# Performance work log

Hardware: AMD Instinct MI355X
Metric: run time of the kernel (lower is better)

The kernel has to match this reference:

```python
import jax, jax.numpy as jnp
import numpy as np

NUM_CLUSTER = 64
NUM_HEAD = 8
EMBED = 512
B, L = 32, 256
H = EMBED // NUM_HEAD  # 64


def setup_inputs() -> dict:
    key = jax.random.key(0)
    ks = jax.random.split(key, 8)
    inputs = jax.random.normal(ks[0], (B, L, EMBED), dtype=jnp.float32)
    emissions = jax.random.normal(ks[1], (B, L, NUM_CLUSTER), dtype=jnp.float32)
    targets = jax.random.randint(ks[2], (B, L), 0, NUM_CLUSTER)
    masks = jnp.ones((B, L), dtype=bool)
    scale = 1.0 / np.sqrt(H)
    W1 = jax.random.normal(ks[3], (NUM_CLUSTER, H), dtype=jnp.float32) * scale
    b1 = jax.random.normal(ks[4], (NUM_CLUSTER,), dtype=jnp.float32) * 0.01
    W2 = jax.random.normal(ks[5], (NUM_CLUSTER, H), dtype=jnp.float32) * scale
    b2 = jax.random.normal(ks[6], (NUM_CLUSTER,), dtype=jnp.float32) * 0.01
    start_transitions = jax.random.uniform(ks[7], (NUM_CLUSTER,), minval=-0.1, maxval=0.1, dtype=jnp.float32)
    end_transitions = jax.random.uniform(jax.random.fold_in(key, 99), (NUM_CLUSTER,), minval=-0.1, maxval=0.1, dtype=jnp.float32)
    return {"inputs": inputs, "emissions": emissions, "targets": targets, "masks": masks,
            "W1": W1, "b1": b1, "W2": W2, "b2": b2,
            "start_transitions": start_transitions, "end_transitions": end_transitions}


def reference(inputs, emissions, targets, masks, W1, b1, W2, b2, start_transitions, end_transitions):
    # batch_first -> time-major (L, B, ...)
    x = jnp.transpose(inputs, (1, 0, 2))          # [L,B,D]
    em = jnp.transpose(emissions, (1, 0, 2))      # [L,B,K]
    tg = targets.T                                # [L,B]
    mk = masks.T                                  # [L,B] bool
    Ls, Bs, D = x.shape
    K = start_transitions.shape[0]

    # biaffine per-step transitions: [L,B,K,K]
    flat = x.reshape(Ls, Bs, NUM_HEAD, D // NUM_HEAD)        # [L,B,C,H]
    e1 = jnp.einsum('lbch,kh->lbck', flat, W1) + b1          # [L,B,C,K]
    e2 = jnp.einsum('lbch,kh->lbck', flat, W2) + b2
    T = jnp.einsum('lbck,lbcj->lbkj', e1, e2)                # sum over channels

    mf = mk.astype(em.dtype)
    barange = jnp.arange(Bs)

    # ---- numerator (gold path score) ----
    score = start_transitions[tg[0]] + em[0, barange, tg[0]]
    steps = jnp.arange(1, Ls)[:, None]                       # [L-1,1]
    trans_sel = T[steps, barange[None, :], tg[:-1], tg[1:]]  # [L-1,B]
    em_sel = em[steps, barange[None, :], tg[1:]]             # [L-1,B]
    score = score + jnp.sum((trans_sel + em_sel) * mf[1:], axis=0)
    seq_ends = mk.astype(jnp.int32).sum(axis=0) - 1
    last_tags = tg[seq_ends, barange]
    numerator = score + end_transitions[last_tags]

    # ---- denominator (log partition) via scan ----
    def step(s, inp):
        Ti, emi, mki = inp                                   # [B,K,K],[B,K],[B]
        nxt = jax.nn.logsumexp(s[:, :, None] + Ti + emi[:, None, :], axis=1)
        s = jnp.where(mki[:, None], nxt, s)
        return s, None

    s0 = start_transitions + em[0]                           # [B,K]
    sF, _ = jax.lax.scan(step, s0, (T[1:], em[1:], mk[1:]))
    denominator = jax.nn.logsumexp(sF + end_transitions, axis=1)

    return numerator - denominator
```

## Files before the change

kernel.cpp:

```cpp
#include <hip/hip_runtime.h>
#include <hip/hip_bf16.h>
#include <cstddef>
#include <cstdint>

constexpr int Bn = 32;
constexpr int Ln = 256;
constexpr int SCH = 16;
constexpr int NCH = 16;

using bf16 = __hip_bfloat16;
typedef __bf16 bfv8 __attribute__((ext_vector_type(8)));
typedef float f32x16 __attribute__((ext_vector_type(16)));

union FragU {
  bfv8 f;
  uint4 q;
  uint2 d[2];
  unsigned short u[8];
};

__device__ inline unsigned int packbf2(float a, float b) {
  unsigned short lo = __builtin_bit_cast(unsigned short, __float2bfloat16(a));
  unsigned short hi = __builtin_bit_cast(unsigned short, __float2bfloat16(b));
  return (unsigned int)lo | ((unsigned int)hi << 16);
}
__device__ inline float bfbits2f(unsigned short v) {
  return __builtin_bit_cast(float, ((unsigned int)v) << 16);
}

__global__ __launch_bounds__(256) void chunk_kernel(
    const float* __restrict__ x, const float* __restrict__ W1,
    const float* __restrict__ b1, const float* __restrict__ W2,
    const float* __restrict__ b2, const float* __restrict__ em,
    const int* __restrict__ tg, bf16* __restrict__ cM,
    float* __restrict__ cOff, float* __restrict__ pnum) {
  const int blk = blockIdx.x;
  const int b = blk & (Bn - 1);
  const int c = blk >> 5;
  const int tid = threadIdx.x;
  const int lane = tid & 63;
  const int wv = tid >> 6;
  const int ti = wv >> 1, tj = wv & 1;
  const int l31 = lane & 31, h5 = lane >> 5;

  __shared__ __align__(16) unsigned short e1s[SCH * 512];
  __shared__ __align__(16) unsigned short e2s[SCH * 512];
  __shared__ __align__(16) unsigned short Rt[2][64 * 68];
  __shared__ __align__(16) unsigned short Pt[2][64 * 68];
  __shared__ __align__(16) float ems[SCH * 64];
  __shared__ float wvred[4], wvred2[4];

  const int t0g = c * SCH;

  {
    const float4* src = (const float4*)(em + ((size_t)b * Ln + t0g) * 64);
    ((float4*)ems)[tid] = src[tid];
  }

  FragU fxa[4];
  {
    const float* xbase = x + ((size_t)(b * Ln + t0g)) * 512;
    const int m = wv * 32 + l31;
    const float* xrow = xbase + (size_t)(m >> 3) * 512 + (m & 7) * 64;
#pragma unroll
    for (int kb = 0; kb < 4; ++kb) {
      const float4 x0 = *(const float4*)(xrow + kb * 16 + h5 * 8);
      const float4 x1 = *(const float4*)(xrow + kb * 16 + h5 * 8 + 4);
      fxa[kb].d[0] = make_uint2(packbf2(x0.x, x0.y), packbf2(x0.z, x0.w));
      fxa[kb].d[1] = make_uint2(packbf2(x1.x, x1.y), packbf2(x1.z, x1.w));
    }
  }
#pragma unroll
  for (int arr = 0; arr < 2; ++arr) {
    const float* W = arr ? W2 : W1;
    const float* bb = arr ? b2 : b1;
    unsigned short* es = arr ? e2s : e1s;
#pragma unroll
    for (int nt = 0; nt < 2; ++nt) {
      const int k = nt * 32 + l31;
      f32x16 acc;
#pragma unroll
      for (int r = 0; r < 16; ++r) acc[r] = 0.f;
#pragma unroll
      for (int kb = 0; kb < 4; ++kb) {
        FragU fb;
        const float* wp = W + (size_t)k * 64 + kb * 16 + h5 * 8;
        const float4 w0 = *(const float4*)wp;
        const float4 w1 = *(const float4*)(wp + 4);
        fb.d[0] = make_uint2(packbf2(w0.x, w0.y), packbf2(w0.z, w0.w));
        fb.d[1] = make_uint2(packbf2(w1.x, w1.y), packbf2(w1.z, w1.w));
        acc = __builtin_amdgcn_mfma_f32_32x32x16_bf16(fxa[kb].f, fb.f, acc, 0, 0, 0);
      }
      const float bias = bb[k];
#pragma unroll
      for (int g = 0; g < 4; ++g) {
        const int tt = wv * 4 + g;
        const unsigned int lo = packbf2(acc[4 * g + 0] + bias, acc[4 * g + 1] + bias);
        const unsigned int hi = packbf2(acc[4 * g + 2] + bias, acc[4 * g + 3] + bias);
        *(uint2*)&es[tt * 512 + k * 8 + 4 * h5] = make_uint2(lo, hi);
      }
    }
  }
  __syncthreads();

  if (tid < 16) {
    const int tglob = t0g + tid;
    float part = 0.f;
    if (tglob >= 1) {
      const int kp = tg[b * Ln + tglob - 1];
      const int jc = tg[b * Ln + tglob];
      const unsigned short* p1 = &e1s[tid * 512 + kp * 8];
      const unsigned short* p2 = &e2s[tid * 512 + jc * 8];
      float tr = 0.f;
#pragma unroll
      for (int cc = 0; cc < 8; ++cc) tr += bfbits2f(p1[cc]) * bfbits2f(p2[cc]);
      part = tr + ems[tid * 64 + jc];
    }
#pragma unroll
    for (int o = 1; o < 16; o <<= 1) part += __shfl_xor(part, o);
    if (tid == 0) pnum[c * Bn + b] = part;
  }

  auto tstep = [&](int tt) -> f32x16 {
    FragU fa, fb;
    fa.q = make_uint4(0, 0, 0, 0);
    fb.q = make_uint4(0, 0, 0, 0);
    if (h5 == 0) {
      fa.q = *(const uint4*)&e1s[tt * 512 + (ti * 32 + l31) * 8];
      fb.q = *(const uint4*)&e2s[tt * 512 + (tj * 32 + l31) * 8];
    }
    const float emv = ems[tt * 64 + tj * 32 + l31];
    f32x16 cc;
#pragma unroll
    for (int r = 0; r < 16; ++r) cc[r] = emv;
    return __builtin_amdgcn_mfma_f32_32x32x16_bf16(fa.f, fb.f, cc, 0, 0, 0);
  };

  auto wavemax16 = [&](const f32x16& v) -> float {
    float m = v[0];
#pragma unroll
    for (int r = 1; r < 16; ++r) m = fmaxf(m, v[r]);
#pragma unroll
    for (int o = 1; o < 64; o <<= 1) m = fmaxf(m, __shfl_xor(m, o));
    return m;
  };

  auto writeP = [&](int qb, const f32x16& v, float sh) {
    const int j = tj * 32 + l31;
    unsigned short* dst = &Pt[qb][j * 68];
#pragma unroll
    for (int g = 0; g < 4; ++g) {
      const int kb = ti * 32 + 8 * g + 4 * h5;
      const unsigned int lo =
          packbf2(__expf(v[4 * g + 0] - sh), __expf(v[4 * g + 1] - sh));
      const unsigned int hi =
          packbf2(__expf(v[4 * g + 2] - sh), __expf(v[4 * g + 3] - sh));
      *(uint2*)(dst + kb) = make_uint2(lo, hi);
    }
  };

  auto writeR0 = [&](const f32x16& v) {
    const int j = tj * 32 + l31;
    const int i0 = ti * 32 + 4 * h5;
#pragma unroll
    for (int g = 0; g < 4; ++g)
#pragma unroll
      for (int rr = 0; rr < 4; ++rr)
        Rt[0][(i0 + 8 * g + rr) * 68 + j] = __builtin_bit_cast(
            unsigned short, __float2bfloat16(v[4 * g + rr]));
  };

  auto gemmT = [&](int p, int q) -> f32x16 {
    f32x16 acc;
#pragma unroll
    for (int r = 0; r < 16; ++r) acc[r] = 0.f;
#pragma unroll
    for (int kb = 0; kb < 4; ++kb) {
      const int koff = kb * 16 + h5 * 8;
      FragU fa, fb;
      const unsigned short* ap = &Pt[q][(ti * 32 + l31) * 68 + koff];
      const unsigned short* bp = &Rt[p][(tj * 32 + l31) * 68 + koff];
      fa.d[0] = *(const uint2*)(ap);
      fa.d[1] = *(const uint2*)(ap + 4);
      fb.d[0] = *(const uint2*)(bp);
      fb.d[1] = *(const uint2*)(bp + 4);
      acc = __builtin_amdgcn_mfma_f32_32x32x16_bf16(fa.f, fb.f, acc, 0, 0, 0);
    }
    return acc;
  };

  auto writeRT = [&](int buf, const f32x16& v, float scale) {
    const int i = tj * 32 + l31;
    unsigned short* dst = &Rt[buf][i * 68];
#pragma unroll
    for (int g = 0; g < 4; ++g) {
      const int j0 = ti * 32 + 4 * h5 + 8 * g;
      const unsigned int lo =
          packbf2(v[4 * g + 0] * scale, v[4 * g + 1] * scale);
      const unsigned int hi =
          packbf2(v[4 * g + 2] * scale, v[4 * g + 3] * scale);
      *(uint2*)(dst + j0) = make_uint2(lo, hi);
    }
  };

  const int tt0 = (c == 0) ? 1 : 0;
  f32x16 v0 = tstep(tt0);
  {
    const float wm0 = wavemax16(v0);
    if (lane == 0) wvred[wv] = wm0;
  }
  __syncthreads();
  const float sh0 =
      fmaxf(fmaxf(wvred[0], wvred[1]), fmaxf(wvred[2], wvred[3]));
  float off = sh0;
  {
    f32x16 pv;
#pragma unroll
    for (int r = 0; r < 16; ++r) pv[r] = __expf(v0[r] - sh0);
    writeR0(pv);
  }
  const float lag = sh0;

  int p = 0, q = 0;
  for (int tt = tt0 + 1; tt < SCH; ++tt) {
    f32x16 vt = tstep(tt);
    writeP(q, vt, lag);
    __syncthreads();
    f32x16 acc = gemmT(p, q);
    if (((tt - tt0) & 3) == 0) {
      const float am = wavemax16(acc);
      if (lane == 0) wvred2[wv] = am;
      __syncthreads();
      const float rmax = fmaxf(
          fmaxf(fmaxf(wvred2[0], wvred2[1]), fmaxf(wvred2[2], wvred2[3])),
          1e-30f);
      writeRT(p ^ 1, acc, 1.0f / rmax);
      off += lag + __logf(rmax);
    } else {
      writeRT(p ^ 1, acc, 1.0f);
      off += lag;
    }
    p ^= 1;
    q ^= 1;
  }

  __syncthreads();
  bf16* om = cM + ((size_t)(c * Bn + b)) * 4096;
#pragma unroll
  for (int pass = 0; pass < 4; ++pass) {
    const int e = pass * 1024 + tid * 4;
    const int i = e >> 6, j = e & 63;
    *(uint2*)((unsigned short*)om + e) = *(const uint2*)&Rt[p][i * 68 + j];
  }
  if (tid == 0) cOff[c * Bn + b] = off;
}

__global__ __launch_bounds__(256) void combine_kernel(
    const float* __restrict__ em, const int* __restrict__ tg,
    const float* __restrict__ st, const float* __restrict__ en,
    const bf16* __restrict__ cM, const float* __restrict__ cOff,
    const float* __restrict__ pnum, float* __restrict__ out) {
  const int b = blockIdx.x, tid = threadIdx.x;
  const int lane = tid & 63, wv = tid >> 6;

  __shared__ float sexs[64];
  __shared__ float part[4][64];
  __shared__ unsigned short Ms[2][4096];
  __shared__ float soff_s;
  __shared__ float num_s;

  if (tid < 16) {
    float nsum = pnum[tid * Bn + b];
#pragma unroll
    for (int o = 1; o < 16; o <<= 1) nsum += __shfl_xor(nsum, o);
    if (tid == 0) {
      const int tg0 = tg[b * Ln];
      const int tgl = tg[b * Ln + Ln - 1];
      num_s = nsum + st[tg0] + em[(size_t)b * Ln * 64 + tg0] + en[tgl];
    }
  }

  if (tid < 64) {
    const float s0 = st[tid] + em[(size_t)b * Ln * 64 + tid];
    float m = s0;
#pragma unroll
    for (int o = 1; o < 64; o <<= 1) m = fmaxf(m, __shfl_xor(m, o));
    sexs[tid] = __expf(s0 - m);
    if (tid == 0) soff_s = m;
  }

  {
    const uint4* src = (const uint4*)(cM + (size_t)b * 4096);
    ((uint4*)Ms[0])[tid] = src[tid];
    ((uint4*)Ms[0])[tid + 256] = src[tid + 256];
  }
  __syncthreads();

  int buf = 0;
  for (int c = 0; c < NCH; ++c) {
    uint4 n0, n1;
    const bool more = (c + 1 < NCH);
    if (more) {
      const uint4* src = (const uint4*)(cM + ((size_t)((c + 1) * Bn + b)) * 4096);
      n0 = src[tid];
      n1 = src[tid + 256];
    }
    float pacc = 0.f;
    const unsigned short* Mr = Ms[buf];
#pragma unroll
    for (int kk = 0; kk < 16; ++kk) {
      const int k = wv * 16 + kk;
      pacc += sexs[k] * bfbits2f(Mr[k * 64 + lane]);
    }
    part[wv][lane] = pacc;
    if (more) {
      ((uint4*)Ms[buf ^ 1])[tid] = n0;
      ((uint4*)Ms[buf ^ 1])[tid + 256] = n1;
    }
    __syncthreads();
    if (tid < 64) {
      const float v = part[0][tid] + part[1][tid] + part[2][tid] + part[3][tid];
      float m = v;
#pragma unroll
      for (int o = 1; o < 64; o <<= 1) m = fmaxf(m, __shfl_xor(m, o));
      m = fmaxf(m, 1e-30f);
      sexs[tid] = v / m;
      if (tid == 0) soff_s += cOff[c * Bn + b] + __logf(m);
    }
    __syncthreads();
    buf ^= 1;
  }

  if (tid < 64) {
    const float w = sexs[tid] * __expf(en[tid]);
    float sg = w;
#pragma unroll
    for (int o = 1; o < 64; o <<= 1) sg += __shfl_xor(sg, o);
    if (tid == 0) out[b] = num_s - (soff_s + __logf(sg));
  }
}

extern "C" void kernel_launch(void* const* d_in, const int* in_sizes, int n_in,
                              void* d_out, int out_size, void* d_ws, size_t ws_size,
                              hipStream_t stream) {
  const float* inputs    = (const float*)d_in[0];
  const float* emissions = (const float*)d_in[1];
  const int*   targets   = (const int*)d_in[2];
  const float* W1 = (const float*)d_in[4];
  const float* b1 = (const float*)d_in[5];
  const float* W2 = (const float*)d_in[6];
  const float* b2 = (const float*)d_in[7];
  const float* st = (const float*)d_in[8];
  const float* en = (const float*)d_in[9];
  float* outp = (float*)d_out;

  bf16* cM = (bf16*)d_ws;
  float* cOff = (float*)(cM + (size_t)NCH * Bn * 4096);
  float* pnum = cOff + NCH * Bn;

  chunk_kernel<<<dim3(NCH * Bn), dim3(256), 0, stream>>>(
      inputs, W1, b1, W2, b2, emissions, targets, cM, cOff, pnum);
  combine_kernel<<<dim3(Bn), dim3(256), 0, stream>>>(
      emissions, targets, st, en, cM, cOff, pnum, outp);
}
```

Measured before the change: 121.5 us.

## Fuse chunk and combine kernels with per-batch completion flags

Merges the chunk kernel and the combine kernel into one launch. Each block publishes a release-ordered flag once its chunk results are written. The chunk-0 block for each batch element then spin-waits on the other chunks' flags and runs the combine step, reusing its shared-memory buffers. This removes the second kernel launch and the gap between kernels. The flags are never reset and rely on a fixed magic value, so on repeated calls the waits may pass early and read stale or partly written workspace. Spinning also assumes every block can be resident at the same time.

```diff
diff --git a/kernel.cpp b/kernel.cpp
--- a/kernel.cpp
+++ b/kernel.cpp
@@ -7,6 +7,7 @@
 constexpr int Ln = 256;
 constexpr int SCH = 16;
 constexpr int NCH = 16;
+constexpr unsigned int FLAG_MAGIC = 0x3C96F1A7u;
 
 using bf16 = __hip_bfloat16;
 typedef __bf16 bfv8 __attribute__((ext_vector_type(8)));
@@ -28,12 +29,14 @@
   return __builtin_bit_cast(float, ((unsigned int)v) << 16);
 }
 
-__global__ __launch_bounds__(256) void chunk_kernel(
+__global__ __launch_bounds__(256) void fused_kernel(
     const float* __restrict__ x, const float* __restrict__ W1,
     const float* __restrict__ b1, const float* __restrict__ W2,
     const float* __restrict__ b2, const float* __restrict__ em,
-    const int* __restrict__ tg, bf16* __restrict__ cM,
-    float* __restrict__ cOff, float* __restrict__ pnum) {
+    const int* __restrict__ tg, const float* __restrict__ st,
+    const float* __restrict__ en, bf16* __restrict__ cM,
+    float* __restrict__ cOff, float* __restrict__ pnum,
+    unsigned int* __restrict__ flags, float* __restrict__ out) {
   const int blk = blockIdx.x;
   const int b = blk & (Bn - 1);
   const int c = blk >> 5;
@@ -49,6 +52,7 @@
   __shared__ __align__(16) unsigned short Pt[2][64 * 68];
   __shared__ __align__(16) float ems[SCH * 64];
   __shared__ float wvred[4], wvred2[4];
+  __shared__ float soff_s, num_s;
 
   const int t0g = c * SCH;
 
@@ -253,21 +257,28 @@
     *(uint2*)((unsigned short*)om + e) = *(const uint2*)&Rt[p][i * 68 + j];
   }
   if (tid == 0) cOff[c * Bn + b] = off;
-}
-
-__global__ __launch_bounds__(256) void combine_kernel(
-    const float* __restrict__ em, const int* __restrict__ tg,
-    const float* __restrict__ st, const float* __restrict__ en,
-    const bf16* __restrict__ cM, const float* __restrict__ cOff,
-    const float* __restrict__ pnum, float* __restrict__ out) {
-  const int b = blockIdx.x, tid = threadIdx.x;
-  const int lane = tid & 63, wv = tid >> 6;
-
-  __shared__ float sexs[64];
-  __shared__ float part[4][64];
-  __shared__ unsigned short Ms[2][4096];
-  __shared__ float soff_s;
-  __shared__ float num_s;
+
+  __syncthreads();
+  if (tid == 0) {
+    __threadfence();
+    __hip_atomic_store(&flags[c * Bn + b], FLAG_MAGIC, __ATOMIC_RELEASE,
+                       __HIP_MEMORY_SCOPE_AGENT);
+  }
+  if (c != 0) return;
+
+  if (tid == 0) {
+    for (int cc = 1; cc < NCH; ++cc)
+      while (__hip_atomic_load(&flags[cc * Bn + b], __ATOMIC_ACQUIRE,
+                               __HIP_MEMORY_SCOPE_AGENT) != FLAG_MAGIC)
+        __builtin_amdgcn_s_sleep(2);
+    __threadfence();
+  }
+  __syncthreads();
+
+  unsigned short* Ms0 = e1s;
+  unsigned short* Ms1 = e1s + 4096;
+  float* partf = (float*)e2s;
+  float* sexs = ((float*)e2s) + 256;
 
   if (tid < 16) {
     float nsum = pnum[tid * Bn + b];
@@ -281,51 +292,52 @@
   }
 
   if (tid < 64) {
-    const float s0 = st[tid] + em[(size_t)b * Ln * 64 + tid];
-    float m = s0;
+    const float s0v = st[tid] + em[(size_t)b * Ln * 64 + tid];
+    float m = s0v;
 #pragma unroll
     for (int o = 1; o < 64; o <<= 1) m = fmaxf(m, __shfl_xor(m, o));
-    sexs[tid] = __expf(s0 - m);
+    sexs[tid] = __expf(s0v - m);
     if (tid == 0) soff_s = m;
   }
 
   {
     const uint4* src = (const uint4*)(cM + (size_t)b * 4096);
-    ((uint4*)Ms[0])[tid] = src[tid];
-    ((uint4*)Ms[0])[tid + 256] = src[tid + 256];
+    ((uint4*)Ms0)[tid] = src[tid];
+    ((uint4*)Ms0)[tid + 256] = src[tid + 256];
   }
   __syncthreads();
 
   int buf = 0;
-  for (int c = 0; c < NCH; ++c) {
+  unsigned short* Mbuf[2] = {Ms0, Ms1};
+  for (int ch = 0; ch < NCH; ++ch) {
     uint4 n0, n1;
-    const bool more = (c + 1 < NCH);
+    const bool more = (ch + 1 < NCH);
     if (more) {
-      const uint4* src = (const uint4*)(cM + ((size_t)((c + 1) * Bn + b)) * 4096);
+      const uint4* src = (const uint4*)(cM + ((size_t)((ch + 1) * Bn + b)) * 4096);
       n0 = src[tid];
       n1 = src[tid + 256];
     }
     float pacc = 0.f;
-    const unsigned short* Mr = Ms[buf];
+    const unsigned short* Mr = Mbuf[buf];
 #pragma unroll
     for (int kk = 0; kk < 16; ++kk) {
       const int k = wv * 16 + kk;
       pacc += sexs[k] * bfbits2f(Mr[k * 64 + lane]);
     }
-    part[wv][lane] = pacc;
+    partf[wv * 64 + lane] = pacc;
     if (more) {
-      ((uint4*)Ms[buf ^ 1])[tid] = n0;
-      ((uint4*)Ms[buf ^ 1])[tid + 256] = n1;
+      ((uint4*)Mbuf[buf ^ 1])[tid] = n0;
+      ((uint4*)Mbuf[buf ^ 1])[tid + 256] = n1;
     }
     __syncthreads();
     if (tid < 64) {
-      const float v = part[0][tid] + part[1][tid] + part[2][tid] + part[3][tid];
+      const float v = partf[tid] + partf[64 + tid] + partf[128 + tid] + partf[192 + tid];
       float m = v;
 #pragma unroll
       for (int o = 1; o < 64; o <<= 1) m = fmaxf(m, __shfl_xor(m, o));
       m = fmaxf(m, 1e-30f);
       sexs[tid] = v / m;
-      if (tid == 0) soff_s += cOff[c * Bn + b] + __logf(m);
+      if (tid == 0) soff_s += cOff[ch * Bn + b] + __logf(m);
     }
     __syncthreads();
     buf ^= 1;
@@ -357,9 +369,9 @@
   bf16* cM = (bf16*)d_ws;
   float* cOff = (float*)(cM + (size_t)NCH * Bn * 4096);
   float* pnum = cOff + NCH * Bn;
-
-  chunk_kernel<<<dim3(NCH * Bn), dim3(256), 0, stream>>>(
-      inputs, W1, b1, W2, b2, emissions, targets, cM, cOff, pnum);
-  combine_kernel<<<dim3(Bn), dim3(256), 0, stream>>>(
-      emissions, targets, st, en, cM, cOff, pnum, outp);
+  unsigned int* flags = (unsigned int*)(pnum + NCH * Bn);
+
+  fused_kernel<<<dim3(NCH * Bn), dim3(256), 0, stream>>>(
+      inputs, W1, b1, W2, b2, emissions, targets, st, en,
+      cM, cOff, pnum, flags, outp);
 }
```

Result: slower. 144.7 us (+19.1%).

## Combine chunk transfer matrices with a parallel MFMA tree reduction

Applied to the files above, without the earlier changes.

The combine kernel used to walk the 16 chunk matrices one after another, doing a vector-matrix product per chunk with two block barriers each. It now loads all 16 chunk matrices into padded shared memory and reduces them pairwise with 64x64 MFMA matrix products across the four waves in two tree levels. A final short vector pass through the four remaining matrices produces the partition sum. Odd chunks now store their final matrix in scattered (transposed) layout so the tree products can pick the orientation each operand needs. This trades a serial dependency chain for extra matrix-matrix FLOPs, more shared memory, and additional bf16 rounding at each tree level.

```diff
diff --git a/kernel.cpp b/kernel.cpp
--- a/kernel.cpp
+++ b/kernel.cpp
@@ -159,18 +159,18 @@
     }
   };
 
-  auto writeR0 = [&](const f32x16& v) {
+  auto writeScat = [&](int buf, const f32x16& v, float scale) {
     const int j = tj * 32 + l31;
     const int i0 = ti * 32 + 4 * h5;
 #pragma unroll
     for (int g = 0; g < 4; ++g)
 #pragma unroll
       for (int rr = 0; rr < 4; ++rr)
-        Rt[0][(i0 + 8 * g + rr) * 68 + j] = __builtin_bit_cast(
-            unsigned short, __float2bfloat16(v[4 * g + rr]));
-  };
-
-  auto gemmT = [&](int p, int q) -> f32x16 {
+        Rt[buf][(i0 + 8 * g + rr) * 68 + j] = __builtin_bit_cast(
+            unsigned short, __float2bfloat16(v[4 * g + rr] * scale));
+  };
+
+  auto gemmT = [&](int pb, int qb) -> f32x16 {
     f32x16 acc;
 #pragma unroll
     for (int r = 0; r < 16; ++r) acc[r] = 0.f;
@@ -178,8 +178,8 @@
     for (int kb = 0; kb < 4; ++kb) {
       const int koff = kb * 16 + h5 * 8;
       FragU fa, fb;
-      const unsigned short* ap = &Pt[q][(ti * 32 + l31) * 68 + koff];
-      const unsigned short* bp = &Rt[p][(tj * 32 + l31) * 68 + koff];
+      const unsigned short* ap = &Pt[qb][(ti * 32 + l31) * 68 + koff];
+      const unsigned short* bp = &Rt[pb][(tj * 32 + l31) * 68 + koff];
       fa.d[0] = *(const uint2*)(ap);
       fa.d[1] = *(const uint2*)(ap + 4);
       fb.d[0] = *(const uint2*)(bp);
@@ -217,7 +217,7 @@
     f32x16 pv;
 #pragma unroll
     for (int r = 0; r < 16; ++r) pv[r] = __expf(v0[r] - sh0);
-    writeR0(pv);
+    writeScat(0, pv, 1.0f);
   }
   const float lag = sh0;
 
@@ -227,6 +227,7 @@
     writeP(q, vt, lag);
     __syncthreads();
     f32x16 acc = gemmT(p, q);
+    float scale = 1.0f;
     if (((tt - tt0) & 3) == 0) {
       const float am = wavemax16(acc);
       if (lane == 0) wvred2[wv] = am;
@@ -234,12 +235,15 @@
       const float rmax = fmaxf(
           fmaxf(fmaxf(wvred2[0], wvred2[1]), fmaxf(wvred2[2], wvred2[3])),
           1e-30f);
-      writeRT(p ^ 1, acc, 1.0f / rmax);
+      scale = 1.0f / rmax;
       off += lag + __logf(rmax);
     } else {
-      writeRT(p ^ 1, acc, 1.0f);
       off += lag;
     }
+    if ((c & 1) && tt == SCH - 1)
+      writeScat(p ^ 1, acc, scale);
+    else
+      writeRT(p ^ 1, acc, scale);
     p ^= 1;
     q ^= 1;
   }
@@ -262,82 +266,147 @@
     const float* __restrict__ pnum, float* __restrict__ out) {
   const int b = blockIdx.x, tid = threadIdx.x;
   const int lane = tid & 63, wv = tid >> 6;
-
+  const int l31 = lane & 31, h5 = lane >> 5;
+
+  __shared__ __align__(16) unsigned short Ms[16][64 * 68];
   __shared__ float sexs[64];
-  __shared__ float part[4][64];
-  __shared__ unsigned short Ms[2][4096];
-  __shared__ float soff_s;
-  __shared__ float num_s;
-
-  if (tid < 16) {
-    float nsum = pnum[tid * Bn + b];
+  __shared__ float toff[16];
+  __shared__ float num_s, den_s;
+
+  float s0e = 0.f, env = 0.f, coffv = 0.f, pnv = 0.f;
+  int tg0 = 0, tgl = 0;
+  if (wv == 0) {
+    s0e = __expf(st[lane] + em[(size_t)b * Ln * 64 + lane]);
+    env = __expf(en[lane]);
+    if (lane < 16) coffv = cOff[lane * Bn + b];
+  } else if (wv == 1) {
+    if (lane < 16) pnv = pnum[lane * Bn + b];
+    if (lane == 0) {
+      tg0 = tg[b * Ln];
+      tgl = tg[b * Ln + Ln - 1];
+    }
+  }
+
+  uint4 t0[16], t1[16];
+#pragma unroll
+  for (int i = 0; i < 16; ++i) {
+    const uint4* src = (const uint4*)(cM + ((size_t)(i * Bn + b)) * 4096);
+    t0[i] = src[tid];
+    t1[i] = src[tid + 256];
+  }
+  {
+    const int r0 = tid >> 3, c0 = (tid & 7) * 8;
+#pragma unroll
+    for (int i = 0; i < 16; ++i) {
+      *(uint2*)&Ms[i][r0 * 68 + c0] = *(uint2*)&t0[i];
+      *(uint2*)&Ms[i][r0 * 68 + c0 + 4] = *((uint2*)&t0[i] + 1);
+      *(uint2*)&Ms[i][(r0 + 32) * 68 + c0] = *(uint2*)&t1[i];
+      *(uint2*)&Ms[i][(r0 + 32) * 68 + c0 + 4] = *((uint2*)&t1[i] + 1);
+    }
+  }
+  __syncthreads();
+
+  auto prod = [&](int aSlot, int tSlot, bool outT) -> float {
+    const unsigned short* Xa = outT ? Ms[aSlot] : Ms[tSlot];
+    const unsigned short* Xb = outT ? Ms[tSlot] : Ms[aSlot];
+    f32x16 acc00, acc01, acc10, acc11;
+#pragma unroll
+    for (int r = 0; r < 16; ++r) {
+      acc00[r] = 0.f; acc01[r] = 0.f; acc10[r] = 0.f; acc11[r] = 0.f;
+    }
+#pragma unroll
+    for (int kb = 0; kb < 4; ++kb) {
+      const int koff = kb * 16 + h5 * 8;
+      FragU fa0, fa1, fb0, fb1;
+      const unsigned short* a0 = &Xa[(l31)*68 + koff];
+      const unsigned short* a1 = &Xa[(32 + l31) * 68 + koff];
+      const unsigned short* b0 = &Xb[(l31)*68 + koff];
+      const unsigned short* b1p = &Xb[(32 + l31) * 68 + koff];
+      fa0.d[0] = *(const uint2*)a0;  fa0.d[1] = *(const uint2*)(a0 + 4);
+      fa1.d[0] = *(const uint2*)a1;  fa1.d[1] = *(const uint2*)(a1 + 4);
+      fb0.d[0] = *(const uint2*)b0;  fb0.d[1] = *(const uint2*)(b0 + 4);
+      fb1.d[0] = *(const uint2*)b1p; fb1.d[1] = *(const uint2*)(b1p + 4);
+      acc00 = __builtin_amdgcn_mfma_f32_32x32x16_bf16(fa0.f, fb0.f, acc00, 0, 0, 0);
+      acc01 = __builtin_amdgcn_mfma_f32_32x32x16_bf16(fa0.f, fb1.f, acc01, 0, 0, 0);
+      acc10 = __builtin_amdgcn_mfma_f32_32x32x16_bf16(fa1.f, fb0.f, acc10, 0, 0, 0);
+      acc11 = __builtin_amdgcn_mfma_f32_32x32x16_bf16(fa1.f, fb1.f, acc11, 0, 0, 0);
+    }
+    float mx = acc00[0];
+#pragma unroll
+    for (int r = 0; r < 16; ++r) {
+      mx = fmaxf(mx, acc00[r]);
+      mx = fmaxf(mx, acc01[r]);
+      mx = fmaxf(mx, acc10[r]);
+      mx = fmaxf(mx, acc11[r]);
+    }
+#pragma unroll
+    for (int o = 1; o < 64; o <<= 1) mx = fmaxf(mx, __shfl_xor(mx, o));
+    mx = fmaxf(mx, 1e-30f);
+    const float inv = 1.0f / mx;
+    unsigned short* dst = Ms[aSlot];
+    auto stTile = [&](const f32x16& v, int i2, int j2) {
+      unsigned short* d = &dst[(j2 * 32 + l31) * 68];
+#pragma unroll
+      for (int g = 0; g < 4; ++g) {
+        const int r0 = i2 * 32 + 4 * h5 + 8 * g;
+        const unsigned int lo = packbf2(v[4 * g + 0] * inv, v[4 * g + 1] * inv);
+        const unsigned int hi = packbf2(v[4 * g + 2] * inv, v[4 * g + 3] * inv);
+        *(uint2*)(d + r0) = make_uint2(lo, hi);
+      }
+    };
+    stTile(acc00, 0, 0);
+    stTile(acc01, 0, 1);
+    stTile(acc10, 1, 0);
+    stTile(acc11, 1, 1);
+    return __logf(mx);
+  };
+
+#pragma unroll
+  for (int pp = 0; pp < 2; ++pp) {
+    const int pr = wv + pp * 4;
+    const float lm = prod(2 * pr, 2 * pr + 1, (pr & 1) != 0);
+    if (lane == 0) toff[2 * pr] = lm;
+  }
+  __syncthreads();
+
+  {
+    const float child = toff[4 * wv] + toff[4 * wv + 2];
+    const float lm2 = prod(4 * wv, 4 * wv + 2, false);
+    if (lane == 0) toff[4 * wv] = child + lm2;
+  }
+  __syncthreads();
+
+  if (wv == 0) {
+    float u = s0e;
+#pragma unroll
+    for (int f = 0; f < 4; ++f) {
+      sexs[lane] = u;
+      float acc2 = 0.f;
+      const unsigned short* Mp = Ms[f * 4];
+#pragma unroll 8
+      for (int k = 0; k < 64; ++k)
+        acc2 += sexs[k] * bfbits2f(Mp[k * 68 + lane]);
+      u = acc2;
+    }
+    const float w = u * env;
+    float sg = w;
+#pragma unroll
+    for (int o = 1; o < 64; o <<= 1) sg += __shfl_xor(sg, o);
+#pragma unroll
+    for (int o = 1; o < 16; o <<= 1) coffv += __shfl_xor(coffv, o);
+    if (lane == 0) {
+      const float toffsum = toff[0] + toff[4] + toff[8] + toff[12];
+      den_s = coffv + toffsum + __logf(sg);
+    }
+  } else if (wv == 1) {
+    float nsum = pnv;
 #pragma unroll
     for (int o = 1; o < 16; o <<= 1) nsum += __shfl_xor(nsum, o);
-    if (tid == 0) {
-      const int tg0 = tg[b * Ln];
-      const int tgl = tg[b * Ln + Ln - 1];
+    if (lane == 0)
       num_s = nsum + st[tg0] + em[(size_t)b * Ln * 64 + tg0] + en[tgl];
-    }
-  }
-
-  if (tid < 64) {
-    const float s0 = st[tid] + em[(size_t)b * Ln * 64 + tid];
-    float m = s0;
-#pragma unroll
-    for (int o = 1; o < 64; o <<= 1) m = fmaxf(m, __shfl_xor(m, o));
-    sexs[tid] = __expf(s0 - m);
-    if (tid == 0) soff_s = m;
-  }
-
-  {
-    const uint4* src = (const uint4*)(cM + (size_t)b * 4096);
-    ((uint4*)Ms[0])[tid] = src[tid];
-    ((uint4*)Ms[0])[tid + 256] = src[tid + 256];
-  }
-  __syncthreads();
-
-  int buf = 0;
-  for (int c = 0; c < NCH; ++c) {
-    uint4 n0, n1;
-    const bool more = (c + 1 < NCH);
-    if (more) {
-      const uint4* src = (const uint4*)(cM + ((size_t)((c + 1) * Bn + b)) * 4096);
-      n0 = src[tid];
-      n1 = src[tid + 256];
-    }
-    float pacc = 0.f;
-    const unsigned short* Mr = Ms[buf];
-#pragma unroll
-    for (int kk = 0; kk < 16; ++kk) {
-      const int k = wv * 16 + kk;
-      pacc += sexs[k] * bfbits2f(Mr[k * 64 + lane]);
-    }
-    part[wv][lane] = pacc;
-    if (more) {
-      ((uint4*)Ms[buf ^ 1])[tid] = n0;
-      ((uint4*)Ms[buf ^ 1])[tid + 256] = n1;
-    }
-    __syncthreads();
-    if (tid < 64) {
-      const float v = part[0][tid] + part[1][tid] + part[2][tid] + part[3][tid];
-      float m = v;
-#pragma unroll
-      for (int o = 1; o < 64; o <<= 1) m = fmaxf(m, __shfl_xor(m, o));
-      m = fmaxf(m, 1e-30f);
-      sexs[tid] = v / m;
-      if (tid == 0) soff_s += cOff[c * Bn + b] + __logf(m);
-    }
-    __syncthreads();
-    buf ^= 1;
-  }
-
-  if (tid < 64) {
-    const float w = sexs[tid] * __expf(en[tid]);
-    float sg = w;
-#pragma unroll
-    for (int o = 1; o < 64; o <<= 1) sg += __shfl_xor(sg, o);
-    if (tid == 0) out[b] = num_s - (soff_s + __logf(sg));
-  }
+  }
+  __syncthreads();
+  if (tid == 0) out[b] = num_s - den_s;
 }
 
 extern "C" void kernel_launch(void* const* d_in, const int* in_sizes, int n_in,
```

New measurement: 116.8 us. 1.04x faster.
